# Optimization experiments

Measured on AMD Instinct MI355X. Metric: run time of the kernel, lower is better.

Reference implementation:

```python
import jax, jax.numpy as jnp
import numpy as np

N_NODES = 50000
N_EDGES = 800000


def _gcn_conv(x, src, dst, norm, W, b, num_nodes):
    # x: [N, Fin] -> h: [N, Fout]; messages gathered from src, scattered to dst.
    h = x @ W
    msgs = h[src] * norm[:, None]                      # [E+N, Fout]
    out = jax.ops.segment_sum(msgs, dst, num_segments=num_nodes)
    return out + b


def _gcn_norm(edge_index, num_nodes):
    # Add self-loops and compute symmetric normalization D^-1/2 (A+I) D^-1/2.
    loops = jnp.arange(num_nodes, dtype=edge_index.dtype)
    src = jnp.concatenate([edge_index[0], loops])
    dst = jnp.concatenate([edge_index[1], loops])
    ones = jnp.ones(src.shape[0], dtype=jnp.float32)
    deg = jax.ops.segment_sum(ones, dst, num_segments=num_nodes)
    dinv = jnp.where(deg > 0, jax.lax.rsqrt(jnp.maximum(deg, 1.0)), 0.0)
    norm = dinv[src] * dinv[dst]
    return src, dst, norm


def setup_inputs() -> dict:
    key = jax.random.key(0)
    k1, k2, k3, k4 = jax.random.split(key, 4)
    map_x = jax.random.normal(k1, (N_NODES, 128), dtype=jnp.float32)
    edge_index = jax.random.randint(k2, (2, N_EDGES), 0, N_NODES, dtype=jnp.int64)
    W1 = jax.random.normal(k3, (128, 64), dtype=jnp.float32) * (1.0 / np.sqrt(128))
    b1 = jnp.zeros((64,), dtype=jnp.float32)
    W2 = jax.random.normal(k4, (64, 32), dtype=jnp.float32) * (1.0 / np.sqrt(64))
    b2 = jnp.zeros((32,), dtype=jnp.float32)
    return {"map": map_x, "edge_index": edge_index, "W1": W1, "b1": b1, "W2": W2, "b2": b2}


def reference(map, edge_index, W1, b1, W2, b2):
    num_nodes = map.shape[0]
    src, dst, norm = _gcn_norm(edge_index, num_nodes)
    x = jax.nn.relu(_gcn_conv(map, src, dst, norm, W1, b1, num_nodes))
    x = jax.nn.relu(_gcn_conv(x, src, dst, norm, W2, b2, num_nodes))
    return x
```

## Files before the change

### kernel.cpp

```cpp
#include <hip/hip_runtime.h>

#define TPB 256
#define ACHUNK 4096
#define BSHIFT 6
#define BNODES 64
#define CAP 2048
#define GROWS 128

__device__ __forceinline__ float blo(unsigned u) { return __uint_as_float(u << 16); }
__device__ __forceinline__ float bhi(unsigned u) { return __uint_as_float(u & 0xffff0000u); }
__device__ __forceinline__ unsigned pack2(float a, float b) {
    unsigned ua = __float_as_uint(a); ua += 0x7fffu + ((ua >> 16) & 1u);
    unsigned ub = __float_as_uint(b); ub += 0x7fffu + ((ub >> 16) & 1u);
    return (ua >> 16) | (ub & 0xffff0000u);
}
__device__ __forceinline__ void dec8(uint4 v, float* f) {
    f[0] = blo(v.x); f[1] = bhi(v.x); f[2] = blo(v.y); f[3] = bhi(v.y);
    f[4] = blo(v.z); f[5] = bhi(v.z); f[6] = blo(v.w); f[7] = bhi(v.w);
}
__device__ __forceinline__ void dec4(uint2 v, float* f) {
    f[0] = blo(v.x); f[1] = bhi(v.x); f[2] = blo(v.y); f[3] = bhi(v.y);
}


__global__ __launch_bounds__(TPB) void k_fat(
        const int* __restrict__ src, const int* __restrict__ dst, int E,
        int* __restrict__ bcnt, int* __restrict__ tmp, int NB,
        const float* __restrict__ X, const float* __restrict__ W,
        unsigned int* __restrict__ H1b, int N, int G1, int FB) {
    __shared__ float Ws[128 * 64];
    int* lcnt = (int*)Ws;
    int bid = blockIdx.x;
    int t = threadIdx.x;

    if ((bid % 3) == 0) {
        int fidx = bid / 3;
        if (fidx >= FB) return;
        int c0 = fidx * ACHUNK;
        int s_[16], d_[16];
#pragma unroll
        for (int i = 0; i < 16; i++) {
            int e = c0 + i * TPB + t;
            if (e < E) { s_[i] = src[e]; d_[i] = dst[e]; }
            else d_[i] = -1;
        }
        for (int b = t; b < NB; b += TPB) lcnt[b] = 0;
        __syncthreads();
#pragma unroll
        for (int i = 0; i < 16; i++)
            if (d_[i] >= 0) atomicAdd(&lcnt[d_[i] >> BSHIFT], 1);
        __syncthreads();
        for (int b = t; b < NB; b += TPB) {
            int c = lcnt[b];
            lcnt[b] = c ? (b * CAP + atomicAdd(&bcnt[b], c)) : 0;
        }
        __syncthreads();
#pragma unroll
        for (int i = 0; i < 16; i++) {
            if (d_[i] >= 0) {
                int bkt = d_[i] >> BSHIFT;
                int pos = atomicAdd(&lcnt[bkt], 1);
                if (pos < (bkt + 1) * CAP) {
                    tmp[pos] = ((d_[i] & (BNODES - 1)) << 16) | s_[i];
                }
            }
        }
    } else {
        int gb = bid - bid / 3 - 1;
        if (gb >= G1) return;
        int row0 = gb * GROWS;

        const float4* W4 = (const float4*)W;
        float4* Ws4 = (float4*)Ws;
#pragma unroll
        for (int i = 0; i < 8; i++) Ws4[t + i * 256] = W4[t + i * 256];
        __syncthreads();

        int rg = t >> 3;
        int c0 = (t & 7) * 8;
        int r0 = row0 + rg * 4;
        int ri[4];
#pragma unroll
        for (int i = 0; i < 4; i++) ri[i] = (r0 + i < N) ? (r0 + i) : (N - 1);

        float acc[4][8];
#pragma unroll
        for (int i = 0; i < 4; i++)
#pragma unroll
            for (int j = 0; j < 8; j++) acc[i][j] = 0.0f;

        const float4* X4 = (const float4*)X;
        for (int kk = 0; kk < 32; kk++) {
            float4 xv[4];
#pragma unroll
            for (int i = 0; i < 4; i++) xv[i] = X4[(size_t)ri[i] * 32 + kk];
#pragma unroll
            for (int q = 0; q < 4; q++) {
                const float* w = Ws + (4 * kk + q) * 64 + c0;
                float wq[8];
#pragma unroll
                for (int j = 0; j < 8; j++) wq[j] = w[j];
                float xq[4];
                xq[0] = q == 0 ? xv[0].x : q == 1 ? xv[0].y : q == 2 ? xv[0].z : xv[0].w;
                xq[1] = q == 0 ? xv[1].x : q == 1 ? xv[1].y : q == 2 ? xv[1].z : xv[1].w;
                xq[2] = q == 0 ? xv[2].x : q == 1 ? xv[2].y : q == 2 ? xv[2].z : xv[2].w;
                xq[3] = q == 0 ? xv[3].x : q == 1 ? xv[3].y : q == 2 ? xv[3].z : xv[3].w;
#pragma unroll
                for (int i = 0; i < 4; i++)
#pragma unroll
                    for (int j = 0; j < 8; j++)
                        acc[i][j] = fmaf(xq[i], wq[j], acc[i][j]);
            }
        }
#pragma unroll
        for (int i = 0; i < 4; i++) {
            if (r0 + i < N) {
                uint4 p = { pack2(acc[i][0], acc[i][1]), pack2(acc[i][2], acc[i][3]),
                            pack2(acc[i][4], acc[i][5]), pack2(acc[i][6], acc[i][7]) };
                *(uint4*)(H1b + (size_t)(r0 + i) * 32 + (t & 7) * 4) = p;
            }
        }
    }
}


__global__ __launch_bounds__(TPB) void k_binB(
        const int* __restrict__ bcnt, const int* __restrict__ tmp,
        int* __restrict__ rowptr, unsigned short* __restrict__ rowlen,
        float* __restrict__ dinv, unsigned short* __restrict__ edges,
        const unsigned int* __restrict__ H1b, unsigned int* __restrict__ g1b,
        int N) {
    __shared__ int hist[BNODES];
    __shared__ int cur[BNODES];
    __shared__ int sh[BNODES];
    __shared__ float dl[BNODES];
    int b = blockIdx.x;
    int t = threadIdx.x;
    int node0 = b << BSHIFT;
    int nn = N - node0; if (nn > BNODES) nn = BNODES;
    int cnt = bcnt[b]; if (cnt > CAP) cnt = CAP;
    const int tb = b * CAP;

    if (t < BNODES) hist[t] = 0;
    __syncthreads();
    for (int i = t; i < cnt; i += TPB) atomicAdd(&hist[tmp[tb + i] >> 16], 1);
    __syncthreads();
    if (t < BNODES) sh[t] = hist[t];
    __syncthreads();
    for (int o = 1; o < BNODES; o <<= 1) {
        int x = (t >= o && t < BNODES) ? sh[t - o] : 0;
        __syncthreads();
        if (t < BNODES) sh[t] += x;
        __syncthreads();
    }
    if (t < BNODES) {
        int v = hist[t];
        int excl = sh[t] - v;
        cur[t] = excl;
        float dv = rsqrtf((float)(v + 1));
        dl[t] = dv;
        if (t < nn) {
            dinv[node0 + t] = dv;
            rowptr[node0 + t] = tb + excl;
            rowlen[node0 + t] = (unsigned short)v;
        }
    }
    __syncthreads();
    for (int i = t; i < cnt; i += TPB) {
        int p = tmp[tb + i];
        int pos = atomicAdd(&cur[p >> 16], 1);
        edges[tb + pos] = (unsigned short)(p & 0xffff);
    }
    const uint4* H4 = (const uint4*)H1b;
    uint4* G4 = (uint4*)g1b;
    for (int i = t; i < nn * 8; i += TPB) {
        int r = i >> 3, q = i & 7;
        float dv = dl[r];
        float f[8];
        uint4 hv = H4[(size_t)(node0 + r) * 8 + q];
        dec8(hv, f);
        uint4 p = { pack2(f[0] * dv, f[1] * dv), pack2(f[2] * dv, f[3] * dv),
                    pack2(f[4] * dv, f[5] * dv), pack2(f[6] * dv, f[7] * dv) };
        G4[(size_t)(node0 + r) * 8 + q] = p;
    }
}


__global__ __launch_bounds__(TPB) void k_gg(
        const int* __restrict__ rowptr, const unsigned short* __restrict__ rowlen,
        const unsigned short* __restrict__ edges,
        const unsigned int* __restrict__ g1b,
        const float* __restrict__ dinv, const float* __restrict__ b1,
        const float* __restrict__ W2, unsigned int* __restrict__ g2b, int N) {
    __shared__ float W2s[64 * 32];
    __shared__ float rows[32 * 68];
    __shared__ float dl[32];
    __shared__ int nst[32];
    __shared__ int nlen[32];
    int t = threadIdx.x;
    int node0 = blockIdx.x * 32;
    int nn = N - node0; if (nn > 32) nn = 32;
    if (nn <= 0) return;

    {
        const float4* W4 = (const float4*)W2;
        float4* Wd = (float4*)W2s;
        Wd[t] = W4[t]; Wd[t + 256] = W4[t + 256];
    }
    if (t < nn) {
        dl[t] = dinv[node0 + t];
        nst[t] = rowptr[node0 + t];
        nlen[t] = rowlen[node0 + t];
    }
    __syncthreads();

    const uint4* G4 = (const uint4*)g1b;
    int nl = t >> 3;
    int lane = t & 7;
    if (nl < nn) {
        float acc[8], f[8];
        uint4 sv = G4[(size_t)(node0 + nl) * 8 + lane];
        dec8(sv, acc);
        int base = nst[nl], deg = nlen[nl];
        int j = 0;
        for (; j + 7 < deg; j += 8) {
            uint4 r[8];
#pragma unroll
            for (int u = 0; u < 8; u++)
                r[u] = G4[(size_t)edges[base + j + u] * 8 + lane];
#pragma unroll
            for (int u = 0; u < 8; u++) {
                dec8(r[u], f);
#pragma unroll
                for (int k = 0; k < 8; k++) acc[k] += f[k];
            }
        }
        for (; j < deg; j++) {
            uint4 r0 = G4[(size_t)edges[base + j] * 8 + lane];
            dec8(r0, f);
#pragma unroll
            for (int k = 0; k < 8; k++) acc[k] += f[k];
        }
        float w0 = dl[nl];
        const float4* bb4 = (const float4*)(b1 + lane * 8);
        float4 ba = bb4[0], bc = bb4[1];
        float* rr = rows + nl * 68 + lane * 8;
        rr[0] = fmaxf(fmaf(acc[0], w0, ba.x), 0.0f);
        rr[1] = fmaxf(fmaf(acc[1], w0, ba.y), 0.0f);
        rr[2] = fmaxf(fmaf(acc[2], w0, ba.z), 0.0f);
        rr[3] = fmaxf(fmaf(acc[3], w0, ba.w), 0.0f);
        rr[4] = fmaxf(fmaf(acc[4], w0, bc.x), 0.0f);
        rr[5] = fmaxf(fmaf(acc[5], w0, bc.y), 0.0f);
        rr[6] = fmaxf(fmaf(acc[6], w0, bc.z), 0.0f);
        rr[7] = fmaxf(fmaf(acc[7], w0, bc.w), 0.0f);
    }
    __syncthreads();

    int n = t >> 3;
    int c = t & 7;
    if (n < nn) {
        const float* row = rows + n * 68;
        float a0 = 0.0f, a1 = 0.0f, a2 = 0.0f, a3 = 0.0f;
#pragma unroll 8
        for (int k = 0; k < 64; k++) {
            float rv = row[k];
            const float* w = W2s + k * 32 + 4 * c;
            a0 = fmaf(rv, w[0], a0); a1 = fmaf(rv, w[1], a1);
            a2 = fmaf(rv, w[2], a2); a3 = fmaf(rv, w[3], a3);
        }
        float dv = dl[n];
        uint2 p = { pack2(a0 * dv, a1 * dv), pack2(a2 * dv, a3 * dv) };
        ((uint2*)g2b)[(size_t)(node0 + n) * 8 + c] = p;
    }
}


__global__ __launch_bounds__(TPB) void k_g32(
        const int* __restrict__ rowptr, const unsigned short* __restrict__ rowlen,
        const unsigned short* __restrict__ edges,
        const unsigned int* __restrict__ g2b,
        const float* __restrict__ dinv, const float* __restrict__ b2,
        float* __restrict__ out, int N) {
    __shared__ float dl[32];
    __shared__ int nst[32];
    __shared__ int nlen[32];
    int t = threadIdx.x;
    int node0 = blockIdx.x * 32;
    int nn = N - node0; if (nn > 32) nn = 32;
    if (nn <= 0) return;
    if (t < nn) {
        dl[t] = dinv[node0 + t];
        nst[t] = rowptr[node0 + t];
        nlen[t] = rowlen[node0 + t];
    }
    __syncthreads();

    int nl = t >> 3;
    int lane = t & 7;
    if (nl >= nn) return;

    const uint2* G2 = (const uint2*)g2b;
    float acc[4], f[4];
    uint2 sv = G2[(size_t)(node0 + nl) * 8 + lane];
    dec4(sv, acc);
    int base = nst[nl], deg = nlen[nl];
    int j = 0;
    for (; j + 15 < deg; j += 16) {
        uint2 r[16];
#pragma unroll
        for (int u = 0; u < 16; u++)
            r[u] = G2[(size_t)edges[base + j + u] * 8 + lane];
#pragma unroll
        for (int u = 0; u < 16; u++) {
            dec4(r[u], f);
            acc[0] += f[0]; acc[1] += f[1]; acc[2] += f[2]; acc[3] += f[3];
        }
    }
    for (; j < deg; j++) {
        uint2 r0 = G2[(size_t)edges[base + j] * 8 + lane];
        dec4(r0, f);
        acc[0] += f[0]; acc[1] += f[1]; acc[2] += f[2]; acc[3] += f[3];
    }
    float w0 = dl[nl];
    const float4* bb4 = (const float4*)(b2 + lane * 4);
    float4 ba = bb4[0];
    float4 o0 = { fmaxf(fmaf(acc[0], w0, ba.x), 0.0f),
                  fmaxf(fmaf(acc[1], w0, ba.y), 0.0f),
                  fmaxf(fmaf(acc[2], w0, ba.z), 0.0f),
                  fmaxf(fmaf(acc[3], w0, ba.w), 0.0f) };
    *(float4*)(out + (size_t)(node0 + nl) * 32 + lane * 4) = o0;
}

static inline int cdiv(int a, int b) { return (a + b - 1) / b; }
static inline char* alignup(char* p) { return (char*)(((uintptr_t)p + 255) & ~(uintptr_t)255); }

extern "C" void kernel_launch(void* const* d_in, const int* in_sizes, int n_in,
                              void* d_out, int out_size, void* d_ws, size_t ws_size,
                              hipStream_t stream) {
    const float* x  = (const float*)d_in[0];
    const int*   ei = (const int*)d_in[1];
    const float* W1 = (const float*)d_in[2];
    const float* b1 = (const float*)d_in[3];
    const float* W2 = (const float*)d_in[4];
    const float* b2 = (const float*)d_in[5];
    float* out = (float*)d_out;

    int N = in_sizes[0] / 128;
    int E = in_sizes[1] / 2;
    const int* src = ei;
    const int* dst = ei + E;

    int NB = cdiv(N, BNODES);

    char* p = (char*)d_ws;
    float* dinv  = (float*)p;            p = alignup(p + sizeof(float) * N);
    int* rowptr  = (int*)p;              p = alignup(p + sizeof(int) * N);
    unsigned short* rowlen = (unsigned short*)p;  p = alignup(p + sizeof(short) * N);
    int* bcnt    = (int*)p;              p = alignup(p + sizeof(int) * 1024);
    int* tmp     = (int*)p;              p = alignup(p + sizeof(int) * (size_t)NB * CAP);
    unsigned short* edges = (unsigned short*)p;   p = alignup(p + sizeof(short) * (size_t)NB * CAP);
    unsigned int* h1b = (unsigned int*)p; p = alignup(p + sizeof(short) * (size_t)N * 64);
    unsigned int* g1b = (unsigned int*)p; p = alignup(p + sizeof(short) * (size_t)N * 64);
    unsigned int* g2b = (unsigned int*)p; p = alignup(p + sizeof(short) * (size_t)N * 32);

    dim3 blk(TPB);
    int FB = cdiv(E, ACHUNK);
    int G1 = cdiv(N, GROWS);
    int fat = 1;
    while ((fat + 2) / 3 < FB || fat - (fat + 2) / 3 < G1) fat++;

    hipMemsetAsync(bcnt, 0, sizeof(int) * 1024, stream);
    k_fat<<<fat, blk, 0, stream>>>(src, dst, E, bcnt, tmp, NB,
                                   x, W1, h1b, N, G1, FB);
    k_binB<<<NB, blk, 0, stream>>>(bcnt, tmp, rowptr, rowlen, dinv,
                                   edges, h1b, g1b, N);
    k_gg<<<cdiv(N, 32), blk, 0, stream>>>(rowptr, rowlen, edges, g1b,
                                          dinv, b1, W2, g2b, N);
    k_g32<<<cdiv(N, 32), blk, 0, stream>>>(rowptr, rowlen, edges, g2b,
                                           dinv, b2, out, N);
}
```

Baseline: 151.4 us.

## Fuse all GCN stages into one persistent cooperative kernel with grid syncs

Replaces the four separate kernel launches with one cooperative persistent kernel. Its blocks loop over the work of each stage (edge binning plus the first matmul, CSR build and scaling, layer-1 gather with the second matmul, layer-2 gather) and separate stages with grid.sync. The aim is to remove launch gaps and tail idling between kernels. In exchange, occupancy is limited by the 32KB shared buffer, the fixed grid gives less parallelism per stage, and grid-wide barriers add their own cost. The old multi-kernel path remains as a fallback if the cooperative launch fails.

```diff
diff --git a/kernel.cpp b/kernel.cpp
--- a/kernel.cpp
+++ b/kernel.cpp
@@ -1,4 +1,6 @@
 #include <hip/hip_runtime.h>
+#include <hip/hip_cooperative_groups.h>
+namespace cg = cooperative_groups;
 
 #define TPB 256
 #define ACHUNK 4096
@@ -20,6 +22,304 @@
 }
 __device__ __forceinline__ void dec4(uint2 v, float* f) {
     f[0] = blo(v.x); f[1] = bhi(v.x); f[2] = blo(v.y); f[3] = bhi(v.y);
+}
+
+
+__global__ __launch_bounds__(TPB) void k_fused(
+        const int* __restrict__ src, const int* __restrict__ dst, int E,
+        int* __restrict__ bcnt, int* __restrict__ tmp, int NB,
+        const float* __restrict__ X, const float* __restrict__ W1,
+        unsigned int* __restrict__ h1b, int N, int G1, int FB,
+        int* __restrict__ rowptr, unsigned short* __restrict__ rowlen,
+        float* __restrict__ dinv, unsigned short* __restrict__ edges,
+        unsigned int* __restrict__ g1b, const float* __restrict__ b1,
+        const float* __restrict__ W2, unsigned int* __restrict__ g2b,
+        const float* __restrict__ b2, float* __restrict__ out, int NH) {
+    cg::grid_group grid = cg::this_grid();
+    __shared__ float Ws[8192];
+    int bid = blockIdx.x;
+    int G = gridDim.x;
+    int t = threadIdx.x;
+
+    for (int w = bid; w < FB + G1; w += G) {
+        __syncthreads();
+        if (w < FB) {
+            int* lcnt = (int*)Ws;
+            int c0 = w * ACHUNK;
+            int s_[16], d_[16];
+#pragma unroll
+            for (int i = 0; i < 16; i++) {
+                int e = c0 + i * TPB + t;
+                if (e < E) { s_[i] = src[e]; d_[i] = dst[e]; }
+                else d_[i] = -1;
+            }
+            for (int b = t; b < NB; b += TPB) lcnt[b] = 0;
+            __syncthreads();
+#pragma unroll
+            for (int i = 0; i < 16; i++)
+                if (d_[i] >= 0) atomicAdd(&lcnt[d_[i] >> BSHIFT], 1);
+            __syncthreads();
+            for (int b = t; b < NB; b += TPB) {
+                int c = lcnt[b];
+                lcnt[b] = c ? (b * CAP + atomicAdd(&bcnt[b], c)) : 0;
+            }
+            __syncthreads();
+#pragma unroll
+            for (int i = 0; i < 16; i++) {
+                if (d_[i] >= 0) {
+                    int bkt = d_[i] >> BSHIFT;
+                    int pos = atomicAdd(&lcnt[bkt], 1);
+                    if (pos < (bkt + 1) * CAP) {
+                        tmp[pos] = ((d_[i] & (BNODES - 1)) << 16) | s_[i];
+                    }
+                }
+            }
+        } else {
+            int gb = w - FB;
+            int row0 = gb * GROWS;
+            const float4* W4 = (const float4*)W1;
+            float4* Ws4 = (float4*)Ws;
+#pragma unroll
+            for (int i = 0; i < 8; i++) Ws4[t + i * 256] = W4[t + i * 256];
+            __syncthreads();
+
+            int rg = t >> 3;
+            int c0 = (t & 7) * 8;
+            int r0 = row0 + rg * 4;
+            int ri[4];
+#pragma unroll
+            for (int i = 0; i < 4; i++) ri[i] = (r0 + i < N) ? (r0 + i) : (N - 1);
+            float acc[4][8];
+#pragma unroll
+            for (int i = 0; i < 4; i++)
+#pragma unroll
+                for (int j = 0; j < 8; j++) acc[i][j] = 0.0f;
+            const float4* X4 = (const float4*)X;
+            for (int kk = 0; kk < 32; kk++) {
+                float4 xv[4];
+#pragma unroll
+                for (int i = 0; i < 4; i++) xv[i] = X4[(size_t)ri[i] * 32 + kk];
+#pragma unroll
+                for (int q = 0; q < 4; q++) {
+                    const float* wp = Ws + (4 * kk + q) * 64 + c0;
+                    float wq[8];
+#pragma unroll
+                    for (int j = 0; j < 8; j++) wq[j] = wp[j];
+                    float xq[4];
+                    xq[0] = q == 0 ? xv[0].x : q == 1 ? xv[0].y : q == 2 ? xv[0].z : xv[0].w;
+                    xq[1] = q == 0 ? xv[1].x : q == 1 ? xv[1].y : q == 2 ? xv[1].z : xv[1].w;
+                    xq[2] = q == 0 ? xv[2].x : q == 1 ? xv[2].y : q == 2 ? xv[2].z : xv[2].w;
+                    xq[3] = q == 0 ? xv[3].x : q == 1 ? xv[3].y : q == 2 ? xv[3].z : xv[3].w;
+#pragma unroll
+                    for (int i = 0; i < 4; i++)
+#pragma unroll
+                        for (int j = 0; j < 8; j++)
+                            acc[i][j] = fmaf(xq[i], wq[j], acc[i][j]);
+                }
+            }
+#pragma unroll
+            for (int i = 0; i < 4; i++) {
+                if (r0 + i < N) {
+                    uint4 p = { pack2(acc[i][0], acc[i][1]), pack2(acc[i][2], acc[i][3]),
+                                pack2(acc[i][4], acc[i][5]), pack2(acc[i][6], acc[i][7]) };
+                    *(uint4*)(h1b + (size_t)(r0 + i) * 32 + (t & 7) * 4) = p;
+                }
+            }
+        }
+    }
+    grid.sync();
+
+    for (int b = bid; b < NB; b += G) {
+        __syncthreads();
+        int* hist = (int*)Ws;
+        int* cur  = hist + BNODES;
+        int* shv  = cur + BNODES;
+        float* dl = (float*)(shv + BNODES);
+        int node0 = b << BSHIFT;
+        int nn = N - node0; if (nn > BNODES) nn = BNODES;
+        int cnt = bcnt[b]; if (cnt > CAP) cnt = CAP;
+        const int tb = b * CAP;
+
+        if (t < BNODES) hist[t] = 0;
+        __syncthreads();
+        for (int i = t; i < cnt; i += TPB) atomicAdd(&hist[tmp[tb + i] >> 16], 1);
+        __syncthreads();
+        if (t < BNODES) shv[t] = hist[t];
+        __syncthreads();
+        for (int o = 1; o < BNODES; o <<= 1) {
+            int x = (t >= o && t < BNODES) ? shv[t - o] : 0;
+            __syncthreads();
+            if (t < BNODES) shv[t] += x;
+            __syncthreads();
+        }
+        if (t < BNODES) {
+            int v = hist[t];
+            int excl = shv[t] - v;
+            cur[t] = excl;
+            float dv = rsqrtf((float)(v + 1));
+            dl[t] = dv;
+            if (t < nn) {
+                dinv[node0 + t] = dv;
+                rowptr[node0 + t] = tb + excl;
+                rowlen[node0 + t] = (unsigned short)v;
+            }
+        }
+        __syncthreads();
+        for (int i = t; i < cnt; i += TPB) {
+            int p = tmp[tb + i];
+            int pos = atomicAdd(&cur[p >> 16], 1);
+            edges[tb + pos] = (unsigned short)(p & 0xffff);
+        }
+        const uint4* H4 = (const uint4*)h1b;
+        uint4* G4 = (uint4*)g1b;
+        for (int i = t; i < nn * 8; i += TPB) {
+            int r = i >> 3, q = i & 7;
+            float dv = dl[r];
+            float f[8];
+            uint4 hv = H4[(size_t)(node0 + r) * 8 + q];
+            dec8(hv, f);
+            uint4 p = { pack2(f[0] * dv, f[1] * dv), pack2(f[2] * dv, f[3] * dv),
+                        pack2(f[4] * dv, f[5] * dv), pack2(f[6] * dv, f[7] * dv) };
+            G4[(size_t)(node0 + r) * 8 + q] = p;
+        }
+    }
+    grid.sync();
+
+    {
+        float* W2s  = Ws;
+        float* rows = Ws + 2048;
+        float* dl   = Ws + 2048 + 2176;
+        int* nst    = (int*)(dl + 32);
+        int* nlen   = nst + 32;
+        const float4* W4 = (const float4*)W2;
+        float4* Wd = (float4*)W2s;
+        Wd[t] = W4[t]; Wd[t + 256] = W4[t + 256];
+        __syncthreads();
+
+        const uint4* G4 = (const uint4*)g1b;
+        for (int hb = bid; hb < NH; hb += G) {
+            __syncthreads();
+            int node0 = hb * 32;
+            int nn = N - node0; if (nn > 32) nn = 32;
+            if (t < nn) {
+                dl[t] = dinv[node0 + t];
+                nst[t] = rowptr[node0 + t];
+                nlen[t] = rowlen[node0 + t];
+            }
+            __syncthreads();
+
+            int nl = t >> 3;
+            int lane = t & 7;
+            if (nl < nn) {
+                float acc[8], f[8];
+                uint4 sv = G4[(size_t)(node0 + nl) * 8 + lane];
+                dec8(sv, acc);
+                int base = nst[nl], deg = nlen[nl];
+                int j = 0;
+                for (; j + 7 < deg; j += 8) {
+                    uint4 r[8];
+#pragma unroll
+                    for (int u = 0; u < 8; u++)
+                        r[u] = G4[(size_t)edges[base + j + u] * 8 + lane];
+#pragma unroll
+                    for (int u = 0; u < 8; u++) {
+                        dec8(r[u], f);
+#pragma unroll
+                        for (int k = 0; k < 8; k++) acc[k] += f[k];
+                    }
+                }
+                for (; j < deg; j++) {
+                    uint4 r0 = G4[(size_t)edges[base + j] * 8 + lane];
+                    dec8(r0, f);
+#pragma unroll
+                    for (int k = 0; k < 8; k++) acc[k] += f[k];
+                }
+                float w0 = dl[nl];
+                const float4* bb4 = (const float4*)(b1 + lane * 8);
+                float4 ba = bb4[0], bc = bb4[1];
+                float* rr = rows + nl * 68 + lane * 8;
+                rr[0] = fmaxf(fmaf(acc[0], w0, ba.x), 0.0f);
+                rr[1] = fmaxf(fmaf(acc[1], w0, ba.y), 0.0f);
+                rr[2] = fmaxf(fmaf(acc[2], w0, ba.z), 0.0f);
+                rr[3] = fmaxf(fmaf(acc[3], w0, ba.w), 0.0f);
+                rr[4] = fmaxf(fmaf(acc[4], w0, bc.x), 0.0f);
+                rr[5] = fmaxf(fmaf(acc[5], w0, bc.y), 0.0f);
+                rr[6] = fmaxf(fmaf(acc[6], w0, bc.z), 0.0f);
+                rr[7] = fmaxf(fmaf(acc[7], w0, bc.w), 0.0f);
+            }
+            __syncthreads();
+
+            int n = t >> 3;
+            int c = t & 7;
+            if (n < nn) {
+                const float* row = rows + n * 68;
+                float a0 = 0.0f, a1 = 0.0f, a2 = 0.0f, a3 = 0.0f;
+#pragma unroll 8
+                for (int k = 0; k < 64; k++) {
+                    float rv = row[k];
+                    const float* w = W2s + k * 32 + 4 * c;
+                    a0 = fmaf(rv, w[0], a0); a1 = fmaf(rv, w[1], a1);
+                    a2 = fmaf(rv, w[2], a2); a3 = fmaf(rv, w[3], a3);
+                }
+                float dv = dl[n];
+                uint2 p = { pack2(a0 * dv, a1 * dv), pack2(a2 * dv, a3 * dv) };
+                ((uint2*)g2b)[(size_t)(node0 + n) * 8 + c] = p;
+            }
+        }
+    }
+    grid.sync();
+
+    {
+        float* dl = Ws;
+        int* nst  = (int*)(dl + 32);
+        int* nlen = nst + 32;
+        const uint2* G2 = (const uint2*)g2b;
+        for (int hb = bid; hb < NH; hb += G) {
+            __syncthreads();
+            int node0 = hb * 32;
+            int nn = N - node0; if (nn > 32) nn = 32;
+            if (t < nn) {
+                dl[t] = dinv[node0 + t];
+                nst[t] = rowptr[node0 + t];
+                nlen[t] = rowlen[node0 + t];
+            }
+            __syncthreads();
+
+            int nl = t >> 3;
+            int lane = t & 7;
+            if (nl < nn) {
+                float acc[4], f[4];
+                uint2 sv = G2[(size_t)(node0 + nl) * 8 + lane];
+                dec4(sv, acc);
+                int base = nst[nl], deg = nlen[nl];
+                int j = 0;
+                for (; j + 15 < deg; j += 16) {
+                    uint2 r[16];
+#pragma unroll
+                    for (int u = 0; u < 16; u++)
+                        r[u] = G2[(size_t)edges[base + j + u] * 8 + lane];
+#pragma unroll
+                    for (int u = 0; u < 16; u++) {
+                        dec4(r[u], f);
+                        acc[0] += f[0]; acc[1] += f[1]; acc[2] += f[2]; acc[3] += f[3];
+                    }
+                }
+                for (; j < deg; j++) {
+                    uint2 r0 = G2[(size_t)edges[base + j] * 8 + lane];
+                    dec4(r0, f);
+                    acc[0] += f[0]; acc[1] += f[1]; acc[2] += f[2]; acc[3] += f[3];
+                }
+                float w0 = dl[nl];
+                const float4* bb4 = (const float4*)(b2 + lane * 4);
+                float4 ba = bb4[0];
+                float4 o0 = { fmaxf(fmaf(acc[0], w0, ba.x), 0.0f),
+                              fmaxf(fmaf(acc[1], w0, ba.y), 0.0f),
+                              fmaxf(fmaf(acc[2], w0, ba.z), 0.0f),
+                              fmaxf(fmaf(acc[3], w0, ba.w), 0.0f) };
+                *(float4*)(out + (size_t)(node0 + nl) * 32 + lane * 4) = o0;
+            }
+        }
+    }
 }
 
 
@@ -69,26 +369,22 @@
         int gb = bid - bid / 3 - 1;
         if (gb >= G1) return;
         int row0 = gb * GROWS;
-
         const float4* W4 = (const float4*)W;
         float4* Ws4 = (float4*)Ws;
 #pragma unroll
         for (int i = 0; i < 8; i++) Ws4[t + i * 256] = W4[t + i * 256];
         __syncthreads();
-
         int rg = t >> 3;
         int c0 = (t & 7) * 8;
         int r0 = row0 + rg * 4;
         int ri[4];
 #pragma unroll
         for (int i = 0; i < 4; i++) ri[i] = (r0 + i < N) ? (r0 + i) : (N - 1);
-
         float acc[4][8];
 #pragma unroll
         for (int i = 0; i < 4; i++)
 #pragma unroll
             for (int j = 0; j < 8; j++) acc[i][j] = 0.0f;
-
         const float4* X4 = (const float4*)X;
         for (int kk = 0; kk < 32; kk++) {
             float4 xv[4];
@@ -122,7 +418,6 @@
         }
     }
 }
-
 
 __global__ __launch_bounds__(TPB) void k_binB(
         const int* __restrict__ bcnt, const int* __restrict__ tmp,
@@ -132,7 +427,7 @@
         int N) {
     __shared__ int hist[BNODES];
     __shared__ int cur[BNODES];
-    __shared__ int sh[BNODES];
+    __shared__ int shv[BNODES];
     __shared__ float dl[BNODES];
     int b = blockIdx.x;
     int t = threadIdx.x;
@@ -145,17 +440,17 @@
     __syncthreads();
     for (int i = t; i < cnt; i += TPB) atomicAdd(&hist[tmp[tb + i] >> 16], 1);
     __syncthreads();
-    if (t < BNODES) sh[t] = hist[t];
+    if (t < BNODES) shv[t] = hist[t];
     __syncthreads();
     for (int o = 1; o < BNODES; o <<= 1) {
-        int x = (t >= o && t < BNODES) ? sh[t - o] : 0;
-        __syncthreads();
-        if (t < BNODES) sh[t] += x;
+        int x = (t >= o && t < BNODES) ? shv[t - o] : 0;
+        __syncthreads();
+        if (t < BNODES) shv[t] += x;
         __syncthreads();
     }
     if (t < BNODES) {
         int v = hist[t];
-        int excl = sh[t] - v;
+        int excl = shv[t] - v;
         cur[t] = excl;
         float dv = rsqrtf((float)(v + 1));
         dl[t] = dv;
@@ -184,7 +479,6 @@
         G4[(size_t)(node0 + r) * 8 + q] = p;
     }
 }
-
 
 __global__ __launch_bounds__(TPB) void k_gg(
         const int* __restrict__ rowptr, const unsigned short* __restrict__ rowlen,
@@ -201,7 +495,6 @@
     int node0 = blockIdx.x * 32;
     int nn = N - node0; if (nn > 32) nn = 32;
     if (nn <= 0) return;
-
     {
         const float4* W4 = (const float4*)W2;
         float4* Wd = (float4*)W2s;
@@ -213,7 +506,6 @@
         nlen[t] = rowlen[node0 + t];
     }
     __syncthreads();
-
     const uint4* G4 = (const uint4*)g1b;
     int nl = t >> 3;
     int lane = t & 7;
@@ -255,7 +547,6 @@
         rr[7] = fmaxf(fmaf(acc[7], w0, bc.w), 0.0f);
     }
     __syncthreads();
-
     int n = t >> 3;
     int c = t & 7;
     if (n < nn) {
@@ -273,7 +564,6 @@
         ((uint2*)g2b)[(size_t)(node0 + n) * 8 + c] = p;
     }
 }
-
 
 __global__ __launch_bounds__(TPB) void k_g32(
         const int* __restrict__ rowptr, const unsigned short* __restrict__ rowlen,
@@ -294,11 +584,9 @@
         nlen[t] = rowlen[node0 + t];
     }
     __syncthreads();
-
     int nl = t >> 3;
     int lane = t & 7;
     if (nl >= nn) return;
-
     const uint2* G2 = (const uint2*)g2b;
     float acc[4], f[4];
     uint2 sv = G2[(size_t)(node0 + nl) * 8 + lane];
@@ -351,6 +639,7 @@
     const int* dst = ei + E;
 
     int NB = cdiv(N, BNODES);
+    int NH = cdiv(N, 32);
 
     char* p = (char*)d_ws;
     float* dinv  = (float*)p;            p = alignup(p + sizeof(float) * N);
@@ -366,16 +655,44 @@
     dim3 blk(TPB);
     int FB = cdiv(E, ACHUNK);
     int G1 = cdiv(N, GROWS);
-    int fat = 1;
-    while ((fat + 2) / 3 < FB || fat - (fat + 2) / 3 < G1) fat++;
 
     hipMemsetAsync(bcnt, 0, sizeof(int) * 1024, stream);
-    k_fat<<<fat, blk, 0, stream>>>(src, dst, E, bcnt, tmp, NB,
-                                   x, W1, h1b, N, G1, FB);
-    k_binB<<<NB, blk, 0, stream>>>(bcnt, tmp, rowptr, rowlen, dinv,
-                                   edges, h1b, g1b, N);
-    k_gg<<<cdiv(N, 32), blk, 0, stream>>>(rowptr, rowlen, edges, g1b,
-                                          dinv, b1, W2, g2b, N);
-    k_g32<<<cdiv(N, 32), blk, 0, stream>>>(rowptr, rowlen, edges, g2b,
-                                           dinv, b2, out, N);
-}
+
+    int maxPerCU = 0;
+    hipError_t occErr = hipOccupancyMaxActiveBlocksPerMultiprocessor(
+        &maxPerCU, (const void*)k_fused, TPB, 0);
+    int numCU = 0;
+    int dev = 0;
+    hipGetDevice(&dev);
+    hipDeviceGetAttribute(&numCU, hipDeviceAttributeMultiprocessorCount, dev);
+    int G = (occErr == hipSuccess && maxPerCU > 0 && numCU > 0) ? maxPerCU * numCU : 0;
+    if (G > NH) G = NH;
+
+    bool coop_ok = false;
+    if (G > 0) {
+        void* args[] = { (void*)&src, (void*)&dst, (void*)&E,
+                         (void*)&bcnt, (void*)&tmp, (void*)&NB,
+                         (void*)&x, (void*)&W1, (void*)&h1b,
+                         (void*)&N, (void*)&G1, (void*)&FB,
+                         (void*)&rowptr, (void*)&rowlen, (void*)&dinv,
+                         (void*)&edges, (void*)&g1b, (void*)&b1,
+                         (void*)&W2, (void*)&g2b, (void*)&b2,
+                         (void*)&out, (void*)&NH };
+        hipError_t err = hipLaunchCooperativeKernel((const void*)k_fused,
+                                                    dim3(G), blk, args, 0, stream);
+        coop_ok = (err == hipSuccess);
+    }
+
+    if (!coop_ok) {
+        int fat = 1;
+        while ((fat + 2) / 3 < FB || fat - (fat + 2) / 3 < G1) fat++;
+        k_fat<<<fat, blk, 0, stream>>>(src, dst, E, bcnt, tmp, NB,
+                                       x, W1, h1b, N, G1, FB);
+        k_binB<<<NB, blk, 0, stream>>>(bcnt, tmp, rowptr, rowlen, dinv,
+                                       edges, h1b, g1b, N);
+        k_gg<<<NH, blk, 0, stream>>>(rowptr, rowlen, edges, g1b,
+                                     dinv, b1, W2, g2b, N);
+        k_g32<<<NH, blk, 0, stream>>>(rowptr, rowlen, edges, g2b,
+                                      dinv, b2, out, N);
+    }
+}
```

New measurement: 330.6 us. 118% more time.

## Replace global bucket atomics with per-chunk local bucket sort and offset table

Applied to the files above, without the earlier changes.

Each edge chunk now sorts its edges into buckets locally with a block-wide prefix scan and writes them contiguously into its own chunk region, recording per-chunk bucket offsets, instead of using global atomics on bucket counters. The binning kernel then walks every chunk's offset range for its bucket to build histograms and scatter edges. This removes the memset and global atomic contention but makes each bucket block serially loop over ~196 chunks with small scattered reads, which could be slower. The scatter writes into global memory may also be less coalesced.

```diff
diff --git a/kernel.cpp b/kernel.cpp
--- a/kernel.cpp
+++ b/kernel.cpp
@@ -25,17 +25,19 @@
 
 __global__ __launch_bounds__(TPB) void k_fat(
         const int* __restrict__ src, const int* __restrict__ dst, int E,
-        int* __restrict__ bcnt, int* __restrict__ tmp, int NB,
+        int* __restrict__ offg, int* __restrict__ tmp, int NB,
         const float* __restrict__ X, const float* __restrict__ W,
         unsigned int* __restrict__ H1b, int N, int G1, int FB) {
-    __shared__ float Ws[128 * 64];
-    int* lcnt = (int*)Ws;
+    __shared__ float Ws[8192];
     int bid = blockIdx.x;
     int t = threadIdx.x;
 
     if ((bid % 3) == 0) {
         int fidx = bid / 3;
         if (fidx >= FB) return;
+        int* hist = (int*)Ws;
+        int* hoff = hist + NB;
+        int* part = hoff + NB;
         int c0 = fidx * ACHUNK;
         int s_[16], d_[16];
 #pragma unroll
@@ -44,25 +46,39 @@
             if (e < E) { s_[i] = src[e]; d_[i] = dst[e]; }
             else d_[i] = -1;
         }
-        for (int b = t; b < NB; b += TPB) lcnt[b] = 0;
+        for (int b = t; b < NB; b += TPB) hist[b] = 0;
         __syncthreads();
 #pragma unroll
         for (int i = 0; i < 16; i++)
-            if (d_[i] >= 0) atomicAdd(&lcnt[d_[i] >> BSHIFT], 1);
-        __syncthreads();
-        for (int b = t; b < NB; b += TPB) {
-            int c = lcnt[b];
-            lcnt[b] = c ? (b * CAP + atomicAdd(&bcnt[b], c)) : 0;
-        }
+            if (d_[i] >= 0) atomicAdd(&hist[d_[i] >> BSHIFT], 1);
+        __syncthreads();
+        int base = t * 4;
+        int v[4], tsum = 0;
+#pragma unroll
+        for (int j = 0; j < 4; j++) { v[j] = (base + j < NB) ? hist[base + j] : 0; tsum += v[j]; }
+        part[t] = tsum;
+        __syncthreads();
+        for (int o = 1; o < TPB; o <<= 1) {
+            int x = (t >= o) ? part[t - o] : 0;
+            __syncthreads();
+            part[t] += x;
+            __syncthreads();
+        }
+        int run = part[t] - tsum;
+        const int os = fidx * (NB + 1);
+#pragma unroll
+        for (int j = 0; j < 4; j++) {
+            if (base + j < NB) { hoff[base + j] = run; offg[os + base + j] = run; }
+            run += v[j];
+        }
+        if (t == TPB - 1) offg[os + NB] = part[TPB - 1];
         __syncthreads();
 #pragma unroll
         for (int i = 0; i < 16; i++) {
             if (d_[i] >= 0) {
                 int bkt = d_[i] >> BSHIFT;
-                int pos = atomicAdd(&lcnt[bkt], 1);
-                if (pos < (bkt + 1) * CAP) {
-                    tmp[pos] = ((d_[i] & (BNODES - 1)) << 16) | s_[i];
-                }
+                int pos = atomicAdd(&hoff[bkt], 1);
+                tmp[c0 + pos] = ((d_[i] & (BNODES - 1)) << 16) | s_[i];
             }
         }
     } else {
@@ -125,37 +141,41 @@
 
 
 __global__ __launch_bounds__(TPB) void k_binB(
-        const int* __restrict__ bcnt, const int* __restrict__ tmp,
+        const int* __restrict__ offg, const int* __restrict__ tmp,
         int* __restrict__ rowptr, unsigned short* __restrict__ rowlen,
         float* __restrict__ dinv, unsigned short* __restrict__ edges,
         const unsigned int* __restrict__ H1b, unsigned int* __restrict__ g1b,
-        int N) {
+        int N, int FB, int NB) {
     __shared__ int hist[BNODES];
     __shared__ int cur[BNODES];
-    __shared__ int sh[BNODES];
+    __shared__ int shl[BNODES];
     __shared__ float dl[BNODES];
     int b = blockIdx.x;
     int t = threadIdx.x;
     int node0 = b << BSHIFT;
     int nn = N - node0; if (nn > BNODES) nn = BNODES;
-    int cnt = bcnt[b]; if (cnt > CAP) cnt = CAP;
     const int tb = b * CAP;
 
     if (t < BNODES) hist[t] = 0;
     __syncthreads();
-    for (int i = t; i < cnt; i += TPB) atomicAdd(&hist[tmp[tb + i] >> 16], 1);
-    __syncthreads();
-    if (t < BNODES) sh[t] = hist[t];
+    for (int f = t; f < FB; f += TPB) {
+        int o0 = offg[f * (NB + 1) + b];
+        int o1 = offg[f * (NB + 1) + b + 1];
+        const int* tp = tmp + f * ACHUNK;
+        for (int i = o0; i < o1; i++) atomicAdd(&hist[tp[i] >> 16], 1);
+    }
+    __syncthreads();
+    if (t < BNODES) shl[t] = hist[t];
     __syncthreads();
     for (int o = 1; o < BNODES; o <<= 1) {
-        int x = (t >= o && t < BNODES) ? sh[t - o] : 0;
-        __syncthreads();
-        if (t < BNODES) sh[t] += x;
+        int x = (t >= o && t < BNODES) ? shl[t - o] : 0;
+        __syncthreads();
+        if (t < BNODES) shl[t] += x;
         __syncthreads();
     }
     if (t < BNODES) {
         int v = hist[t];
-        int excl = sh[t] - v;
+        int excl = shl[t] - v;
         cur[t] = excl;
         float dv = rsqrtf((float)(v + 1));
         dl[t] = dv;
@@ -166,10 +186,15 @@
         }
     }
     __syncthreads();
-    for (int i = t; i < cnt; i += TPB) {
-        int p = tmp[tb + i];
-        int pos = atomicAdd(&cur[p >> 16], 1);
-        edges[tb + pos] = (unsigned short)(p & 0xffff);
+    for (int f = t; f < FB; f += TPB) {
+        int o0 = offg[f * (NB + 1) + b];
+        int o1 = offg[f * (NB + 1) + b + 1];
+        const int* tp = tmp + f * ACHUNK;
+        for (int i = o0; i < o1; i++) {
+            int p = tp[i];
+            int pos = atomicAdd(&cur[p >> 16], 1);
+            if (pos < CAP) edges[tb + pos] = (unsigned short)(p & 0xffff);
+        }
     }
     const uint4* H4 = (const uint4*)H1b;
     uint4* G4 = (uint4*)g1b;
@@ -351,29 +376,28 @@
     const int* dst = ei + E;
 
     int NB = cdiv(N, BNODES);
+    int FB = cdiv(E, ACHUNK);
+    int G1 = cdiv(N, GROWS);
 
     char* p = (char*)d_ws;
     float* dinv  = (float*)p;            p = alignup(p + sizeof(float) * N);
     int* rowptr  = (int*)p;              p = alignup(p + sizeof(int) * N);
     unsigned short* rowlen = (unsigned short*)p;  p = alignup(p + sizeof(short) * N);
-    int* bcnt    = (int*)p;              p = alignup(p + sizeof(int) * 1024);
-    int* tmp     = (int*)p;              p = alignup(p + sizeof(int) * (size_t)NB * CAP);
-    unsigned short* edges = (unsigned short*)p;   p = alignup(p + sizeof(short) * (size_t)NB * CAP);
+    int* offg    = (int*)p;              p = alignup(p + sizeof(int) * (size_t)FB * (NB + 1));
+    int* tmp     = (int*)p;              p = alignup(p + sizeof(int) * (size_t)FB * ACHUNK);
+    unsigned short* edges = (unsigned short*)p;   p = alignup(p + sizeof(short) * ((size_t)NB * CAP + 4096));
     unsigned int* h1b = (unsigned int*)p; p = alignup(p + sizeof(short) * (size_t)N * 64);
     unsigned int* g1b = (unsigned int*)p; p = alignup(p + sizeof(short) * (size_t)N * 64);
     unsigned int* g2b = (unsigned int*)p; p = alignup(p + sizeof(short) * (size_t)N * 32);
 
     dim3 blk(TPB);
-    int FB = cdiv(E, ACHUNK);
-    int G1 = cdiv(N, GROWS);
     int fat = 1;
     while ((fat + 2) / 3 < FB || fat - (fat + 2) / 3 < G1) fat++;
 
-    hipMemsetAsync(bcnt, 0, sizeof(int) * 1024, stream);
-    k_fat<<<fat, blk, 0, stream>>>(src, dst, E, bcnt, tmp, NB,
+    k_fat<<<fat, blk, 0, stream>>>(src, dst, E, offg, tmp, NB,
                                    x, W1, h1b, N, G1, FB);
-    k_binB<<<NB, blk, 0, stream>>>(bcnt, tmp, rowptr, rowlen, dinv,
-                                   edges, h1b, g1b, N);
+    k_binB<<<NB, blk, 0, stream>>>(offg, tmp, rowptr, rowlen, dinv,
+                                   edges, h1b, g1b, N, FB, NB);
     k_gg<<<cdiv(N, 32), blk, 0, stream>>>(rowptr, rowlen, edges, g1b,
                                           dinv, b1, W2, g2b, N);
     k_g32<<<cdiv(N, 32), blk, 0, stream>>>(rowptr, rowlen, edges, g2b,
```

Measured after the change: 158.7 us. +4.8%, slower.
